# Kernel optimization log

Hardware: AMD Instinct MI355X
Metric: run time of the kernel (lower is better)

## Reference

```python
import jax, jax.numpy as jnp
import numpy as np

B, S, V, E, H, T = 64, 512, 30000, 300, 256, 9


def _lstm_dir(x, Wih, Whh, bih, bhh, reverse):
    # x: [S,B,E] time-major; PyTorch gate order i,f,g,o
    if reverse:
        x = x[::-1]
    b = bih + bhh
    def step(carry, xt):
        h, c = carry
        g = xt @ Wih.T + h @ Whh.T + b
        i, f, gg, o = jnp.split(g, 4, axis=-1)
        c = jax.nn.sigmoid(f) * c + jax.nn.sigmoid(i) * jnp.tanh(gg)
        h = jax.nn.sigmoid(o) * jnp.tanh(c)
        return (h, c), h
    h0 = jnp.zeros((x.shape[1], H), x.dtype)
    _, hs = jax.lax.scan(step, (h0, h0), x)
    if reverse:
        hs = hs[::-1]
    return hs  # [S,B,H]


def _crf_nll(emissions, tags, mask, start_t, end_t, trans):
    # emissions [B,S,T], tags [B,S] int, mask [B,S] bool; torchcrf math, reduction='sum'
    em = jnp.swapaxes(emissions, 0, 1)                      # [S,B,T]
    tg = jnp.swapaxes(tags, 0, 1)                           # [S,B]
    mk = jnp.swapaxes(mask, 0, 1).astype(emissions.dtype)   # [S,B]
    batch = jnp.arange(emissions.shape[0])
    # numerator: gold path score
    score0 = start_t[tg[0]] + em[0, batch, tg[0]]
    def num_step(score, inp):
        tprev, tcur, emt, mt = inp
        s = trans[tprev, tcur] + emt[batch, tcur]
        return score + mt * s, None
    score, _ = jax.lax.scan(num_step, score0, (tg[:-1], tg[1:], em[1:], mk[1:]))
    seq_ends = jnp.sum(mask, axis=1).astype(jnp.int32) - 1
    last_tags = tags[batch, seq_ends]
    score = score + end_t[last_tags]
    # denominator: forward algorithm (logsumexp over tags per timestep)
    alpha0 = start_t[None, :] + em[0]                       # [B,T]
    def fwd_step(alpha, inp):
        emt, mt = inp
        nxt = jax.nn.logsumexp(alpha[:, :, None] + trans[None] + emt[:, None, :], axis=1)
        alpha = jnp.where(mt[:, None] > 0, nxt, alpha)
        return alpha, None
    alpha, _ = jax.lax.scan(fwd_step, alpha0, (em[1:], mk[1:]))
    logZ = jax.nn.logsumexp(alpha + end_t[None, :], axis=1)
    return -jnp.sum(score - logZ)


def setup_inputs() -> dict:
    key = jax.random.key(0)
    ks = jax.random.split(key, 12)
    sd = jnp.float32(0.08)
    f32 = jnp.float32
    return {
        "input_ids": jax.random.randint(ks[0], (B, S), 0, V),
        "labels": jax.random.randint(ks[1], (B, S), 0, T),
        "attention_mask": jnp.ones((B, S), dtype=bool),
        "emb": jax.random.normal(ks[2], (V, E), f32) * sd,
        "Wih_f": jax.random.normal(ks[3], (4 * H, E), f32) * sd,
        "Whh_f": jax.random.normal(ks[4], (4 * H, H), f32) * sd,
        "bih_f": jnp.zeros((4 * H,), f32),
        "bhh_f": jnp.zeros((4 * H,), f32),
        "Wih_b": jax.random.normal(ks[5], (4 * H, E), f32) * sd,
        "Whh_b": jax.random.normal(ks[6], (4 * H, H), f32) * sd,
        "bih_b": jnp.zeros((4 * H,), f32),
        "bhh_b": jnp.zeros((4 * H,), f32),
        "clf_W": jax.random.normal(ks[7], (T, 2 * H), f32) * sd,
        "clf_b": jnp.zeros((T,), f32),
        "start_t": jax.random.normal(ks[8], (T,), f32) * 0.1,
        "end_t": jax.random.normal(ks[9], (T,), f32) * 0.1,
        "trans": jax.random.normal(ks[10], (T, T), f32) * 0.1,
    }


def reference(input_ids, labels, attention_mask, emb, Wih_f, Whh_f, bih_f, bhh_f, Wih_b, Whh_b, bih_b, bhh_b, clf_W, clf_b, start_t, end_t, trans):
    x = emb[input_ids]                 # [B,S,E] embedding gather (dropout = identity in eval)
    xt = jnp.swapaxes(x, 0, 1)         # [S,B,E]
    h_f = _lstm_dir(xt, Wih_f, Whh_f, bih_f, bhh_f, False)
    h_b = _lstm_dir(xt, Wih_b, Whh_b, bih_b, bhh_b, True)
    h = jnp.concatenate([h_f, h_b], axis=-1)                 # [S,B,2H]
    logits = jnp.swapaxes(h, 0, 1) @ clf_W.T + clf_b         # [B,S,T]
    loss = _crf_nll(logits, labels, attention_mask, start_t, end_t, trans)
    return loss, logits
```

## Files before the change

### kernel.cpp

```cpp
#include <hip/hip_runtime.h>
#include <stdint.h>

typedef float v4f __attribute__((ext_vector_type(4)));
typedef float v2f __attribute__((ext_vector_type(2)));
typedef short bf16x8 __attribute__((ext_vector_type(8)));
typedef int v4i __attribute__((ext_vector_type(4)));
typedef int v8i __attribute__((ext_vector_type(8)));
typedef unsigned int uint32;
typedef unsigned long long u64;

#define V_N 30000
#define E_N 300
#define EPAD 320
#define H_N 256
#define G_N 1024
#define B_N 64
#define S_N 512
#define T_N 9

#define OFF_EMB  ((size_t)0)
#define OFF_WIH  ((size_t)19200000)
#define OFF_WHH  ((size_t)20510720)
#define OFF_PRE  ((size_t)21035008)
#define OFF_H    ((size_t)155252736)

__device__ __forceinline__ uint32 bf16r(float x){
  uint32 u = __float_as_uint(x);
  u += 0x7FFFu + ((u>>16)&1u);
  return u>>16;
}
__device__ __forceinline__ float sigm(float x){
  return __builtin_amdgcn_rcpf(1.f + __builtin_amdgcn_exp2f(-1.4426950408889634f*x));
}
__device__ __forceinline__ float tanh_(float x){
  return 1.f - 2.f*__builtin_amdgcn_rcpf(1.f + __builtin_amdgcn_exp2f(2.8853900817779268f*x));
}

__global__ void k_convert(const float* __restrict__ emb,
                          const float* __restrict__ wih_f,
                          const float* __restrict__ wih_b,
                          char* __restrict__ ws, float* __restrict__ out){
  int tid = blockIdx.x*256 + threadIdx.x;
  if (tid == 0) out[0] = 0.f;
  const int NE = V_N*40;
  unsigned short* eo = (unsigned short*)(ws + OFF_EMB);
  unsigned short* wo = (unsigned short*)(ws + OFF_WIH);
  const float* src; unsigned short* dst; int g;
  if (tid < NE){
    int row = tid/40; g = tid%40;
    src = emb + (size_t)row*E_N;
    dst = eo + (size_t)row*EPAD + g*8;
  } else if (tid < NE + 2*G_N*40){
    int t2 = tid - NE;
    int dir = t2/(G_N*40); int r2 = t2%(G_N*40);
    int row = r2/40; g = r2%40;
    src = (dir? wih_b : wih_f) + (size_t)row*E_N;
    dst = wo + ((size_t)dir*G_N + row)*EPAD + g*8;
  } else return;
  unsigned short v[8];
  #pragma unroll
  for (int j=0;j<8;j++){
    int c = g*8+j;
    float x = (c < E_N)? src[c] : 0.f;
    v[j] = (unsigned short)bf16r(x);
  }
  uint4 pk;
  pk.x = (uint32)v[0] | ((uint32)v[1]<<16);
  pk.y = (uint32)v[2] | ((uint32)v[3]<<16);
  pk.z = (uint32)v[4] | ((uint32)v[5]<<16);
  pk.w = (uint32)v[6] | ((uint32)v[7]<<16);
  *(uint4*)dst = pk;
}

__global__ void k_whh(const float* __restrict__ whh_f, const float* __restrict__ whh_b,
                      char* __restrict__ ws){
  int tid = blockIdx.x*256 + threadIdx.x;
  int part = tid&3;
  int lane = (tid>>2)&63;
  int kk = (tid>>8)&1, tt = (tid>>9)&7, w = (tid>>12)&7, dir = (tid>>15)&1;
  const float* W = dir? whh_b : whh_f;
  int n = lane&15, lq = lane>>4;
  int col = (tt>>1)*256 + w*32 + (tt&1)*16 + n;
  int k0  = kk*128 + lq*32 + part*8;
  const float* p = W + (size_t)col*H_N + k0;
  int lo = __builtin_amdgcn_cvt_pk_fp8_f32(p[0]*64.f, p[1]*64.f, 0, false);
  lo = __builtin_amdgcn_cvt_pk_fp8_f32(p[2]*64.f, p[3]*64.f, lo, true);
  int hi = __builtin_amdgcn_cvt_pk_fp8_f32(p[4]*64.f, p[5]*64.f, 0, false);
  hi = __builtin_amdgcn_cvt_pk_fp8_f32(p[6]*64.f, p[7]*64.f, hi, true);
  u64 v = (uint32)lo | ((u64)(uint32)hi<<32);
  ((u64*)(ws+OFF_WHH))[tid] = v;
}

__global__ __launch_bounds__(256,2)
void k_gemm1(const int* __restrict__ ids, char* __restrict__ ws,
             const float* __restrict__ bih_f, const float* __restrict__ bhh_f,
             const float* __restrict__ bih_b, const float* __restrict__ bhh_b){
  int bx = blockIdx.x;
  int nc = bx & 7, tp = (bx>>3)&255, dir = bx>>11;
  const unsigned short* embb = (const unsigned short*)(ws+OFF_EMB);
  const unsigned short* wihb = (const unsigned short*)(ws+OFF_WIH) + (size_t)dir*G_N*EPAD;
  __shared__ unsigned short Asl[128*32];
  __shared__ unsigned short Bsl[128*32];
  __shared__ int ids_s[128];
  int tid = threadIdx.x, lane = tid&63, w = tid>>6;
  if (tid < 128){
    int t = tp*2 + (tid>>6), b = tid&63;
    ids_s[tid] = ids[b*S_N + t];
  }
  __syncthreads();
  v4f acc[2][8];
  #pragma unroll
  for (int i=0;i<2;i++)
    #pragma unroll
    for (int j=0;j<8;j++) acc[i][j] = (v4f){0.f,0.f,0.f,0.f};
  int r = tid>>1, hf = tid&1;
  int n0 = lane&15, q = lane>>4;
  const float* bi = dir? bih_b : bih_f;
  const float* bh = dir? bhh_b : bhh_f;
  float bv[8];
  #pragma unroll
  for (int nt=0; nt<8; nt++){
    int c = nc*128 + nt*16 + n0;
    bv[nt] = bi[c] + bh[c];
  }
  for (int ks=0; ks<10; ks++){
    const float4* pa = (const float4*)(embb + (size_t)ids_s[r]*EPAD + ks*32 + hf*16);
    float4 a0 = pa[0], a1 = pa[1];
    const float4* pb = (const float4*)(wihb + (size_t)(nc*128 + r)*EPAD + ks*32 + hf*16);
    float4 b0 = pb[0], b1 = pb[1];
    __syncthreads();
    float4* da = (float4*)(Asl + r*32 + hf*16); da[0]=a0; da[1]=a1;
    float4* db = (float4*)(Bsl + r*32 + hf*16); db[0]=b0; db[1]=b1;
    __syncthreads();
    bf16x8 bfr[8], afr[2];
    #pragma unroll
    for (int nt=0; nt<8; nt++) bfr[nt] = *(const bf16x8*)(Bsl + (nt*16+n0)*32 + q*8);
    afr[0] = *(const bf16x8*)(Asl + (w*16+n0)*32 + q*8);
    afr[1] = *(const bf16x8*)(Asl + ((w+4)*16+n0)*32 + q*8);
    #pragma unroll
    for (int mi=0; mi<2; mi++)
      #pragma unroll
      for (int nt=0; nt<8; nt++)
        acc[mi][nt] = __builtin_amdgcn_mfma_f32_16x16x32_bf16(afr[mi], bfr[nt], acc[mi][nt], 0,0,0);
  }
  uint2* pre = (uint2*)(ws + OFF_PRE);
  #pragma unroll
  for (int mi=0; mi<2; mi++){
    int t = tp*2 + mi;
    #pragma unroll
    for (int nt=0; nt<8; nt++){
      int ct = nc*8 + nt;
      size_t tile = (((size_t)(dir*S_N + t)*4 + w)*64 + ct);
      v4f a = acc[mi][nt];
      uint2 o;
      o.x = bf16r(a[0]+bv[nt]) | (bf16r(a[1]+bv[nt])<<16);
      o.y = bf16r(a[2]+bv[nt]) | (bf16r(a[3]+bv[nt])<<16);
      pre[tile*64 + lane] = o;
    }
  }
}

#define MFMA_SC(A,B,C) __builtin_amdgcn_mfma_scale_f32_16x16x128_f8f6f4( \
    (A), (B), (C), 0, 0, 0, 0x7F7F7F7F, 0, 0x75757575)

template<int R0>
__device__ __forceinline__ void lstm_loop(
    const char* pp, int sstride, const int* voff, int ab,
    const v8i (*Wf)[2], float* scw, int n0, bool act,
    char* hb0, char* hb1, int hb_off, float* hp, int hstride,
    int lane, int hw, volatile int* vc, int* ctrs)
{
  uint32 pr[8];
  #pragma unroll
  for (int tt=0;tt<8;tt++) pr[tt] = 0u;
  if (act){
    #pragma unroll
    for (int tt=0;tt<8;tt++) pr[tt] = *(const uint32*)(pp + voff[tt]);
  }
  pp += sstride;
  float c0 = 0.f;
  v4f acc[8];
  #pragma unroll
  for (int tt=0;tt<8;tt++) acc[tt] = (v4f){0.f,0.f,0.f,0.f};
  char* hbr = hb0; char* hbw = hb1;
  int rb = (((lane>>4)&1)*16 + n0)*2 + (lane>>5);
  #pragma unroll 1
  for (int step=0; step<S_N; step++){
    int need = 4*step;
    while (vc[0] < need) __builtin_amdgcn_s_sleep(1);
    v8i afr0, afr1;
    { v4i lo = *(const v4i*)(hbr + ab);       v4i hi = *(const v4i*)(hbr + ab + 16);
      afr0 = __builtin_shufflevector(lo,hi,0,1,2,3,4,5,6,7); }
    if (act){
      #pragma unroll
      for (int tt=0;tt<8;tt++){
        acc[tt][R0]   = __uint_as_float(pr[tt]<<16);
        acc[tt][R0+1] = __uint_as_float(pr[tt] & 0xFFFF0000u);
      }
      #pragma unroll
      for (int tt=0;tt<8;tt++) pr[tt] = *(const uint32*)(pp + voff[tt]);
    }
    pp += sstride;
    #pragma unroll
    for (int tt=0;tt<8;tt++) acc[tt] = MFMA_SC(afr0, Wf[tt][0], acc[tt]);
    while (vc[1] < need) __builtin_amdgcn_s_sleep(1);
    { v4i lo = *(const v4i*)(hbr + ab + 128); v4i hi = *(const v4i*)(hbr + ab + 144);
      afr1 = __builtin_shufflevector(lo,hi,0,1,2,3,4,5,6,7); }
    #pragma unroll
    for (int tt=0;tt<8;tt++) acc[tt] = MFMA_SC(afr1, Wf[tt][1], acc[tt]);
    if (act){
      #pragma unroll
      for (int tt=0;tt<8;tt++){
        int g = tt>>1, uh = tt&1;
        v2f gp = (v2f){ acc[tt][R0], acc[tt][R0+1] };
        *(v2f*)(scw + ((g*2+uh)*16 + n0)*2) = gp;
      }
    }
    float g0 = scw[rb], g1 = scw[rb+64], g2 = scw[rb+128], g3 = scw[rb+192];
    float si = sigm(g0), sf = sigm(g1);
    float tg = tanh_(g2), so = sigm(g3);
    c0 = sf*c0 + si*tg;
    float h = so * tanh_(c0);
    int pk8 = __builtin_amdgcn_cvt_pk_fp8_f32(h*16.f, 0.f, 0, false);
    hbw[hb_off] = (char)(pk8 & 0xFF);
    *hp = h; hp += hstride;
    if (lane == 0) atomicAdd(&ctrs[hw], 1);
    char* t = hbr; hbr = hbw; hbw = t;
  }
}

__global__ __launch_bounds__(512,2)
void k_lstm(char* __restrict__ ws){
  int bx = blockIdx.x;
  int q = bx&7, bg = (bx>>3)&3, dir = bx>>5;
  int tid = threadIdx.x, lane = tid&63, w = tid>>6;
  int n0 = lane&15, lq = lane>>4;
  __shared__ char hbuf[2][16*272];
  __shared__ float gsc[8][256];
  __shared__ int ctrs[2];
  for (int i=tid; i<2176; i+=512) ((int*)hbuf)[i] = 0;
  if (tid < 2) ctrs[tid] = 0;
  const v8i* wp = (const v8i*)(ws + OFF_WHH + (size_t)(dir*8+w)*32768);
  v8i Wf[8][2];
  #pragma unroll
  for (int tt=0; tt<8; tt++)
    #pragma unroll
    for (int kk=0; kk<2; kk++)
      Wf[tt][kk] = wp[(tt*2+kk)*64 + lane];
  int st0 = dir? (S_N-1) : 0;
  const char* pp = ws + OFF_PRE + (size_t)dir*67108864 + (size_t)(st0*4 + bg)*32768;
  const int sstride = dir? -131072 : 131072;
  int voff[8];
  #pragma unroll
  for (int tt=0; tt<8; tt++){
    int g = tt>>1, uh = tt&1;
    int ct = g*16 + w*2 + uh;
    voff[tt] = (ct*64 + lane)*8 + (q&1)*4;
  }
  int ab = n0*272 + lq*32;
  float* scw = gsc[w];
  bool act = (lq == (q>>1));
  int mb = lane>>5, uh0 = (lane>>4)&1;
  int u0 = w*32 + uh0*16 + n0;
  int row = 2*q + mb;
  int hb_off = row*272 + u0;
  float* hout = (float*)(ws+OFF_H);
  int b = bg*16 + row;
  float* hp = hout + ((size_t)b*S_N + st0)*512 + dir*256 + u0;
  const int hstride = dir? -512 : 512;
  int hw = (w >= 4);
  volatile int* vc = (volatile int*)ctrs;
  __syncthreads();
  if (q & 1)
    lstm_loop<2>(pp, sstride, voff, ab, Wf, scw, n0, act, hbuf[0], hbuf[1],
                 hb_off, hp, hstride, lane, hw, vc, ctrs);
  else
    lstm_loop<0>(pp, sstride, voff, ab, Wf, scw, n0, act, hbuf[0], hbuf[1],
                 hb_off, hp, hstride, lane, hw, vc, ctrs);
}

__global__ __launch_bounds__(256)
void k_clf(const char* __restrict__ ws, const float* __restrict__ clfW,
           const float* __restrict__ clfb, float* __restrict__ out){
  int wid = (blockIdx.x*256 + threadIdx.x)>>6;
  int lane = threadIdx.x & 63;
  const float4* h = (const float4*)((const float*)(ws+OFF_H) + (size_t)wid*512);
  float4 h0 = h[lane*2], h1 = h[lane*2+1];
  float a[9];
  #pragma unroll
  for (int t=0;t<9;t++){
    const float4* wp = (const float4*)(clfW + t*512);
    float4 w0 = wp[lane*2], w1 = wp[lane*2+1];
    a[t] = h0.x*w0.x + h0.y*w0.y + h0.z*w0.z + h0.w*w0.w
         + h1.x*w1.x + h1.y*w1.y + h1.z*w1.z + h1.w*w1.w;
  }
  #pragma unroll
  for (int t=0;t<9;t++){
    #pragma unroll
    for (int m=32;m>=1;m>>=1) a[t] += __shfl_xor(a[t], m, 64);
  }
  float val = a[0];
  #pragma unroll
  for (int t=1;t<9;t++) val = (lane==t)? a[t] : val;
  if (lane<9) out[1 + (size_t)wid*9 + lane] = val + clfb[lane];
}

__global__ __launch_bounds__(64)
void k_crf(const int* __restrict__ labels, const float* __restrict__ start_t,
           const float* __restrict__ end_t, const float* __restrict__ trans,
           float* __restrict__ out){
  int b = blockIdx.x, lane = threadIdx.x;
  const float* em = out + 1 + (size_t)b*S_N*T_N;
  const int* tg = labels + (size_t)b*S_N;
  float scv = 0.f;
  for (int t=lane; t<S_N; t+=64){
    int ct = tg[t];
    float e = em[t*T_N + ct];
    if (t==0) scv += start_t[ct] + e;
    else scv += trans[tg[t-1]*T_N + ct] + e;
  }
  if (lane==0) scv += end_t[tg[S_N-1]];
  #pragma unroll
  for (int m=32;m>=1;m>>=1) scv += __shfl_xor(scv, m, 64);
  int j = (lane<9)? lane : 0;
  float wt[9];
  #pragma unroll
  for (int i=0;i<9;i++) wt[i] = trans[i*T_N + j];
  float alpha = start_t[j] + em[j];
  #pragma unroll 1
  for (int t=1;t<S_N;t++){
    float v[9]; float mx = -3.4e38f;
    #pragma unroll
    for (int i=0;i<9;i++){
      float av = __shfl(alpha, i, 64);
      v[i] = av + wt[i];
      mx = fmaxf(mx, v[i]);
    }
    float ss = 0.f;
    #pragma unroll
    for (int i=0;i<9;i++) ss += __builtin_amdgcn_exp2f(1.4426950408889634f*(v[i]-mx));
    alpha = mx + 0.6931471805599453f*__builtin_amdgcn_logf(ss) + em[t*T_N + j];
  }
  float av = (lane<9)? alpha + end_t[j] : -3.4e38f;
  float mx = av;
  #pragma unroll
  for (int m=32;m>=1;m>>=1) mx = fmaxf(mx, __shfl_xor(mx, m, 64));
  float es = (lane<9)? __builtin_amdgcn_exp2f(1.4426950408889634f*(av-mx)) : 0.f;
  #pragma unroll
  for (int m=32;m>=1;m>>=1) es += __shfl_xor(es, m, 64);
  float logZ = mx + 0.6931471805599453f*__builtin_amdgcn_logf(es);
  if (lane==0) atomicAdd(out, logZ - scv);
}

extern "C" void kernel_launch(void* const* d_in, const int* in_sizes, int n_in,
                              void* d_out, int out_size, void* d_ws, size_t ws_size,
                              hipStream_t stream){
  const int* ids      = (const int*)d_in[0];
  const int* labels   = (const int*)d_in[1];
  const float* emb    = (const float*)d_in[3];
  const float* wih_f  = (const float*)d_in[4];
  const float* whh_f  = (const float*)d_in[5];
  const float* bih_f  = (const float*)d_in[6];
  const float* bhh_f  = (const float*)d_in[7];
  const float* wih_b  = (const float*)d_in[8];
  const float* whh_b  = (const float*)d_in[9];
  const float* bih_b  = (const float*)d_in[10];
  const float* bhh_b  = (const float*)d_in[11];
  const float* clfW   = (const float*)d_in[12];
  const float* clfb   = (const float*)d_in[13];
  const float* start_t= (const float*)d_in[14];
  const float* end_t  = (const float*)d_in[15];
  const float* trans  = (const float*)d_in[16];
  float* out = (float*)d_out;
  char* ws = (char*)d_ws;

  hipLaunchKernelGGL(k_convert, dim3((V_N*40 + 2*G_N*40 + 255)/256), dim3(256), 0, stream,
                     emb, wih_f, wih_b, ws, out);
  hipLaunchKernelGGL(k_whh, dim3(256), dim3(256), 0, stream, whh_f, whh_b, ws);
  hipLaunchKernelGGL(k_gemm1, dim3(4096), dim3(256), 0, stream, ids, ws,
                     bih_f, bhh_f, bih_b, bhh_b);
  hipLaunchKernelGGL(k_lstm, dim3(64), dim3(512), 0, stream, ws);
  hipLaunchKernelGGL(k_clf, dim3(8192), dim3(256), 0, stream, ws, clfW, clfb, out);
  hipLaunchKernelGGL(k_crf, dim3(64), dim3(64), 0, stream, labels, start_t, end_t, trans, out);
}
```

Before: 900.1 us.

## Compute LSTM gates in-register with permuted Whh layout, drop LDS gate scatter

```diff
diff --git a/kernel.cpp b/kernel.cpp
--- a/kernel.cpp
+++ b/kernel.cpp
@@ -2,7 +2,6 @@
 #include <stdint.h>
 
 typedef float v4f __attribute__((ext_vector_type(4)));
-typedef float v2f __attribute__((ext_vector_type(2)));
 typedef short bf16x8 __attribute__((ext_vector_type(8)));
 typedef int v4i __attribute__((ext_vector_type(4)));
 typedef int v8i __attribute__((ext_vector_type(8)));
@@ -82,13 +81,20 @@
   int n = lane&15, lq = lane>>4;
   int col = (tt>>1)*256 + w*32 + (tt&1)*16 + n;
   int k0  = kk*128 + lq*32 + part*8;
-  const float* p = W + (size_t)col*H_N + k0;
-  int lo = __builtin_amdgcn_cvt_pk_fp8_f32(p[0]*64.f, p[1]*64.f, 0, false);
-  lo = __builtin_amdgcn_cvt_pk_fp8_f32(p[2]*64.f, p[3]*64.f, lo, true);
-  int hi = __builtin_amdgcn_cvt_pk_fp8_f32(p[4]*64.f, p[5]*64.f, 0, false);
-  hi = __builtin_amdgcn_cvt_pk_fp8_f32(p[6]*64.f, p[7]*64.f, hi, true);
-  u64 v = (uint32)lo | ((u64)(uint32)hi<<32);
-  ((u64*)(ws+OFF_WHH))[tid] = v;
+  const float* p = W + (size_t)col*H_N;
+  float v[8];
+  #pragma unroll
+  for (int j=0;j<8;j++){
+    int pos = k0 + j;
+    int up = (pos & ~31) + ((pos&1)<<4) + ((pos&31)>>1);
+    v[j] = p[up]*64.f;
+  }
+  int lo = __builtin_amdgcn_cvt_pk_fp8_f32(v[0], v[1], 0, false);
+  lo = __builtin_amdgcn_cvt_pk_fp8_f32(v[2], v[3], lo, true);
+  int hi = __builtin_amdgcn_cvt_pk_fp8_f32(v[4], v[5], 0, false);
+  hi = __builtin_amdgcn_cvt_pk_fp8_f32(v[6], v[7], hi, true);
+  u64 vv = (uint32)lo | ((u64)(uint32)hi<<32);
+  ((u64*)(ws+OFF_WHH))[tid] = vv;
 }
 
 __global__ __launch_bounds__(256,2)
@@ -165,67 +171,70 @@
 
 template<int R0>
 __device__ __forceinline__ void lstm_loop(
-    const char* pp, int sstride, const int* voff, int ab,
-    const v8i (*Wf)[2], float* scw, int n0, bool act,
-    char* hb0, char* hb1, int hb_off, float* hp, int hstride,
-    int lane, int hw, volatile int* vc, int* ctrs)
+    const char* __restrict__ pp, int sstride, const int* voff,
+    int ab, const v8i (*Wf)[2], bool act,
+    char* hb0, char* hb1, int hwoff,
+    float* hp, int hstride, int lane, int hw,
+    volatile int* vc, int* ctrs)
 {
   uint32 pr[8];
   #pragma unroll
   for (int tt=0;tt<8;tt++) pr[tt] = 0u;
   if (act){
     #pragma unroll
-    for (int tt=0;tt<8;tt++) pr[tt] = *(const uint32*)(pp + voff[tt]);
+    for (int tt=0;tt<8;tt++) pr[tt] = *(const unsigned short*)(pp + voff[tt]);
   }
   pp += sstride;
-  float c0 = 0.f;
   v4f acc[8];
   #pragma unroll
   for (int tt=0;tt<8;tt++) acc[tt] = (v4f){0.f,0.f,0.f,0.f};
+  float cA = 0.f, cB = 0.f;
+  int need = 0;
   char* hbr = hb0; char* hbw = hb1;
-  int rb = (((lane>>4)&1)*16 + n0)*2 + (lane>>5);
   #pragma unroll 1
-  for (int step=0; step<S_N; step++){
-    int need = 4*step;
-    while (vc[0] < need) __builtin_amdgcn_s_sleep(1);
-    v8i afr0, afr1;
-    { v4i lo = *(const v4i*)(hbr + ab);       v4i hi = *(const v4i*)(hbr + ab + 16);
-      afr0 = __builtin_shufflevector(lo,hi,0,1,2,3,4,5,6,7); }
-    if (act){
+  for (int pair=0; pair<256; pair++){
+    #pragma unroll
+    for (int half=0; half<2; half++){
+      while (vc[0] < need) {}
+      v8i afr0, afr1;
+      { v4i lo = *(const v4i*)(hbr + ab);       v4i hi = *(const v4i*)(hbr + ab + 16);
+        afr0 = __builtin_shufflevector(lo,hi,0,1,2,3,4,5,6,7); }
       #pragma unroll
-      for (int tt=0;tt<8;tt++){
-        acc[tt][R0]   = __uint_as_float(pr[tt]<<16);
-        acc[tt][R0+1] = __uint_as_float(pr[tt] & 0xFFFF0000u);
+      for (int tt=0;tt<8;tt++) acc[tt][R0] = __uint_as_float(pr[tt]<<16);
+      if (act){
+        #pragma unroll
+        for (int tt=0;tt<8;tt++) pr[tt] = *(const unsigned short*)(pp + voff[tt]);
       }
+      pp += sstride;
       #pragma unroll
-      for (int tt=0;tt<8;tt++) pr[tt] = *(const uint32*)(pp + voff[tt]);
+      for (int tt=0;tt<8;tt++) acc[tt] = MFMA_SC(afr0, Wf[tt][0], acc[tt]);
+      while (vc[1] < need) {}
+      { v4i lo = *(const v4i*)(hbr + ab + 128); v4i hi = *(const v4i*)(hbr + ab + 144);
+        afr1 = __builtin_shufflevector(lo,hi,0,1,2,3,4,5,6,7); }
+      #pragma unroll
+      for (int tt=0;tt<8;tt++) acc[tt] = MFMA_SC(afr1, Wf[tt][1], acc[tt]);
+      need += 4;
+      float h0, h1;
+      if (act){
+        float si0 = sigm(acc[0][R0]), sf0 = sigm(acc[2][R0]);
+        float tg0 = tanh_(acc[4][R0]), so0 = sigm(acc[6][R0]);
+        cA = sf0*cA + si0*tg0;
+        h0 = so0 * tanh_(cA);
+        float si1 = sigm(acc[1][R0]), sf1 = sigm(acc[3][R0]);
+        float tg1 = tanh_(acc[5][R0]), so1 = sigm(acc[7][R0]);
+        cB = sf1*cB + si1*tg1;
+        h1 = so1 * tanh_(cB);
+        int pk8 = __builtin_amdgcn_cvt_pk_fp8_f32(h0*16.f, h1*16.f, 0, false);
+        *(unsigned short*)(hbw + hwoff) = (unsigned short)(pk8 & 0xFFFF);
+      }
+      if (lane == 0) atomicAdd(&ctrs[hw], 1);
+      if (act){
+        hp[0]  = h0;
+        hp[16] = h1;
+      }
+      hp += hstride;
+      char* t = hbr; hbr = hbw; hbw = t;
     }
-    pp += sstride;
-    #pragma unroll
-    for (int tt=0;tt<8;tt++) acc[tt] = MFMA_SC(afr0, Wf[tt][0], acc[tt]);
-    while (vc[1] < need) __builtin_amdgcn_s_sleep(1);
-    { v4i lo = *(const v4i*)(hbr + ab + 128); v4i hi = *(const v4i*)(hbr + ab + 144);
-      afr1 = __builtin_shufflevector(lo,hi,0,1,2,3,4,5,6,7); }
-    #pragma unroll
-    for (int tt=0;tt<8;tt++) acc[tt] = MFMA_SC(afr1, Wf[tt][1], acc[tt]);
-    if (act){
-      #pragma unroll
-      for (int tt=0;tt<8;tt++){
-        int g = tt>>1, uh = tt&1;
-        v2f gp = (v2f){ acc[tt][R0], acc[tt][R0+1] };
-        *(v2f*)(scw + ((g*2+uh)*16 + n0)*2) = gp;
-      }
-    }
-    float g0 = scw[rb], g1 = scw[rb+64], g2 = scw[rb+128], g3 = scw[rb+192];
-    float si = sigm(g0), sf = sigm(g1);
-    float tg = tanh_(g2), so = sigm(g3);
-    c0 = sf*c0 + si*tg;
-    float h = so * tanh_(c0);
-    int pk8 = __builtin_amdgcn_cvt_pk_fp8_f32(h*16.f, 0.f, 0, false);
-    hbw[hb_off] = (char)(pk8 & 0xFF);
-    *hp = h; hp += hstride;
-    if (lane == 0) atomicAdd(&ctrs[hw], 1);
-    char* t = hbr; hbr = hbw; hbw = t;
   }
 }
 
@@ -236,7 +245,6 @@
   int tid = threadIdx.x, lane = tid&63, w = tid>>6;
   int n0 = lane&15, lq = lane>>4;
   __shared__ char hbuf[2][16*272];
-  __shared__ float gsc[8][256];
   __shared__ int ctrs[2];
   for (int i=tid; i<2176; i+=512) ((int*)hbuf)[i] = 0;
   if (tid < 2) ctrs[tid] = 0;
@@ -250,33 +258,32 @@
   int st0 = dir? (S_N-1) : 0;
   const char* pp = ws + OFF_PRE + (size_t)dir*67108864 + (size_t)(st0*4 + bg)*32768;
   const int sstride = dir? -131072 : 131072;
+  int R0r = q&3;
   int voff[8];
   #pragma unroll
   for (int tt=0; tt<8; tt++){
     int g = tt>>1, uh = tt&1;
     int ct = g*16 + w*2 + uh;
-    voff[tt] = (ct*64 + lane)*8 + (q&1)*4;
+    voff[tt] = (ct*64 + lane)*8 + R0r*2;
   }
   int ab = n0*272 + lq*32;
-  float* scw = gsc[w];
-  bool act = (lq == (q>>1));
-  int mb = lane>>5, uh0 = (lane>>4)&1;
-  int u0 = w*32 + uh0*16 + n0;
-  int row = 2*q + mb;
-  int hb_off = row*272 + u0;
+  int a = q>>2;
+  bool act = ((lq & 1) == a);
+  int slot = q + (lq & 2)*4;
+  int hwoff = slot*272 + w*32 + n0*2;
   float* hout = (float*)(ws+OFF_H);
-  int b = bg*16 + row;
-  float* hp = hout + ((size_t)b*S_N + st0)*512 + dir*256 + u0;
+  int b = bg*16 + slot;
+  float* hp = hout + ((size_t)b*S_N + st0)*512 + dir*256 + w*32 + n0;
   const int hstride = dir? -512 : 512;
   int hw = (w >= 4);
   volatile int* vc = (volatile int*)ctrs;
   __syncthreads();
-  if (q & 1)
-    lstm_loop<2>(pp, sstride, voff, ab, Wf, scw, n0, act, hbuf[0], hbuf[1],
-                 hb_off, hp, hstride, lane, hw, vc, ctrs);
-  else
-    lstm_loop<0>(pp, sstride, voff, ab, Wf, scw, n0, act, hbuf[0], hbuf[1],
-                 hb_off, hp, hstride, lane, hw, vc, ctrs);
+  switch (R0r){
+    case 0: lstm_loop<0>(pp, sstride, voff, ab, Wf, act, hbuf[0], hbuf[1], hwoff, hp, hstride, lane, hw, vc, ctrs); break;
+    case 1: lstm_loop<1>(pp, sstride, voff, ab, Wf, act, hbuf[0], hbuf[1], hwoff, hp, hstride, lane, hw, vc, ctrs); break;
+    case 2: lstm_loop<2>(pp, sstride, voff, ab, Wf, act, hbuf[0], hbuf[1], hwoff, hp, hstride, lane, hw, vc, ctrs); break;
+    default: lstm_loop<3>(pp, sstride, voff, ab, Wf, act, hbuf[0], hbuf[1], hwoff, hp, hstride, lane, hw, vc, ctrs); break;
+  }
 }
 
 __global__ __launch_bounds__(256)
```

After: 926.4 us. 2.9% more time.
